# Kernel tuning notes

Measured on AMD Instinct MI355X. Metric: run time of the kernel, lower is better.

## Reference

```python
import jax, jax.numpy as jnp
import numpy as np

N_FEATURES = 512
DEPTH = 6
N_TREES = 64
D_OUT = 64
N_LEAVES = 2 ** DEPTH


def setup_inputs() -> dict:
    key = jax.random.key(0)
    k_x, k_w, k_b, k_leaf = jax.random.split(key, 4)
    B = 16384
    x = jax.random.normal(k_x, (B, N_FEATURES), dtype=jnp.float32)
    # depth independent Linear(n_features, n_trees) layers, stacked
    bound = 1.0 / np.sqrt(N_FEATURES)
    W = jax.random.uniform(k_w, (DEPTH, N_FEATURES, N_TREES), dtype=jnp.float32,
                           minval=-bound, maxval=bound)
    b = jax.random.uniform(k_b, (DEPTH, N_TREES), dtype=jnp.float32,
                           minval=-bound, maxval=bound)
    leaf_values = jax.random.normal(k_leaf, (N_TREES, N_LEAVES, D_OUT), dtype=jnp.float32)
    return {"x": x, "W": W, "b": b, "leaf_values": leaf_values}


def reference(x, W, b, leaf_values):
    B = x.shape[0]
    # split probabilities for all levels at once: [B, depth, n_trees]
    split_probs = jax.nn.sigmoid(jnp.einsum('bf,dft->bdt', x, W) + b)
    # bit of leaf index at each level: 0 -> take p (left), 1 -> take 1-p (right)
    leaf_ids = jnp.arange(N_LEAVES)
    # path_probs: [B, n_trees, n_leaves]; small fixed loop over depth levels
    path_probs = jnp.ones((B, N_TREES, N_LEAVES), dtype=x.dtype)
    for level in range(DEPTH):
        bit = (leaf_ids >> (DEPTH - level - 1)) & 1  # [n_leaves]
        p = split_probs[:, level, :, None]           # [B, n_trees, 1]
        path_probs = path_probs * jnp.where(bit == 0, p, 1.0 - p)
    # per-tree leaf combine then mean over trees
    out = jnp.einsum('btl,tld->bd', path_probs, leaf_values) / N_TREES
    return out
```

## Files before the change

### kernel.cpp

```cpp
#include <hip/hip_runtime.h>

#define BATCH   16384
#define NFEAT   512
#define NTREE   64
#define NDEPTH  6
#define NLEAF   64
#define NDOUT   64
#define NLOGIT  384

typedef float    f32x4  __attribute__((ext_vector_type(4)));
typedef short    short8 __attribute__((ext_vector_type(8)));
typedef _Float16 half8  __attribute__((ext_vector_type(8)));
typedef _Float16 h2     __attribute__((ext_vector_type(2)));

union U8 { unsigned short u[8]; short8 v; half8 h; };
union HP { _Float16 h[4]; ushort4 u; };
union HS { _Float16 h; unsigned short s; };
union H8 { h2 p[4]; half8 v; };

__device__ __forceinline__ unsigned short f2bf(float f) {
    union { float f; unsigned int u; } c; c.f = f;
    return (unsigned short)((c.u + 0x8000u) >> 16);
}

__device__ __forceinline__ unsigned short f2h(float f) {
    HS s; s.h = (_Float16)f; return s.s;
}

__device__ __forceinline__ void dma16(const void* g, void* l) {
    __builtin_amdgcn_global_load_lds(
        (const __attribute__((address_space(1))) unsigned int*)g,
        (__attribute__((address_space(3))) unsigned int*)l, 16, 0, 0);
}

__global__ __launch_bounds__(256) void prep(const float* __restrict__ leaf,
                                            const float* __restrict__ W,
                                            unsigned short* __restrict__ V3,
                                            unsigned short* __restrict__ Wt3) {
    __shared__ float T[64 * 65];
    const int tid = threadIdx.x;
    if (blockIdx.x < 64) {
        const int t = blockIdx.x;
        const float* src = leaf + (size_t)t * 4096;
        for (int j = 0; j < 4; ++j) {
            int idx = tid + 256 * j;
            int l = idx >> 4, d4 = idx & 15;
            float4 v = *(const float4*)(src + l * 64 + d4 * 4);
            T[l * 65 + d4 * 4 + 0] = v.x;
            T[l * 65 + d4 * 4 + 1] = v.y;
            T[l * 65 + d4 * 4 + 2] = v.z;
            T[l * 65 + d4 * 4 + 3] = v.w;
        }
        __syncthreads();
        #pragma unroll
        for (int jj = 0; jj < 2; ++jj) {
            int idx = tid + 256 * jj;
            int d = idx >> 3, o = idx & 7;
            int nt = d >> 4, l15 = d & 15;
            int ks = o >> 2, qd = o & 3;
            int lam = qd * 16 + l15;
            U8 u;
            #pragma unroll
            for (int j = 0; j < 8; ++j)
                u.u[j] = f2h(T[(o * 8 + j) * 65 + d] * 0.015625f);
            *(short8*)(V3 + (((size_t)t * 8 + nt * 2 + ks) * 64 + lam) * 8) = u.v;
        }
    } else {
        const int bid = blockIdx.x - 64;
        const int d = bid >> 4, f0 = (bid & 15) * 32;
        for (int j = 0; j < 2; ++j) {
            int idx = tid + 256 * j;
            int f = idx >> 4, c4 = idx & 15;
            float4 v = *(const float4*)(W + ((size_t)d * 512 + f0 + f) * 64 + c4 * 4);
            T[f * 65 + c4 * 4 + 0] = v.x;
            T[f * 65 + c4 * 4 + 1] = v.y;
            T[f * 65 + c4 * 4 + 2] = v.z;
            T[f * 65 + c4 * 4 + 3] = v.w;
        }
        __syncthreads();
        const int t = tid >> 2, c8 = tid & 3;
        U8 u;
        #pragma unroll
        for (int i = 0; i < 8; ++i) u.u[i] = f2bf(T[(c8 * 8 + i) * 65 + t]);
        int k0 = f0 + c8 * 8;
        int kb = k0 >> 6, ks = (k0 >> 5) & 1, qk = (k0 >> 3) & 3;
        int g  = d * 4 + (t >> 4);
        int lam = qk * 16 + (t & 15);
        *(short8*)(Wt3 + (((size_t)kb * 24 + g) * 2 + ks) * 512 + lam * 8) = u.v;
    }
}

__global__ __launch_bounds__(512) void fused(const float* __restrict__ x,
                                             const unsigned short* __restrict__ Wt3,
                                             const float* __restrict__ bias,
                                             const unsigned short* __restrict__ V3,
                                             float* __restrict__ out) {
    __shared__ char SM[64 * 1024];
    _Float16*       sp  = (_Float16*)SM;
    float*          As0 = (float*)(SM + 24 * 1024);
    float*          As1 = (float*)(SM + 32 * 1024);
    _Float16*       red = (_Float16*)(SM + 24 * 1024);

    const int tid  = threadIdx.x;
    const int w = tid >> 6, lane = tid & 63;
    const int quad = lane >> 4, l15 = lane & 15;
    const int r0 = blockIdx.x * 32;
    const int w3 = w * 3;

    f32x4 acc1[2][3];
    #pragma unroll
    for (int mt = 0; mt < 2; ++mt)
        #pragma unroll
        for (int nt = 0; nt < 3; ++nt)
            acc1[mt][nt] = (f32x4){0.f, 0.f, 0.f, 0.f};

    auto stageA = [&](float* buf, int kb) {
        int rl = w * 4 + (lane >> 4);
        const float* g = x + (size_t)(r0 + rl) * NFEAT + kb * 64
                       + (((lane & 15) ^ ((rl & 7) * 2)) * 4);
        dma16(g, (char*)buf + (size_t)w * 1024);
    };
    auto loadBF = [&](int kb, short8 (*bf)[2]) {
        #pragma unroll
        for (int nt = 0; nt < 3; ++nt)
            #pragma unroll
            for (int ks = 0; ks < 2; ++ks)
                bf[nt][ks] = *(const short8*)(Wt3 +
                    (((size_t)kb * 24 + w3 + nt) * 2 + ks) * 512 + lane * 8);
    };
    auto computeStep = [&](const float* buf, short8 (*bf)[2]) {
        short8 aF[2][2];
        #pragma unroll
        for (int mt = 0; mt < 2; ++mt) {
            int r = mt * 16 + l15;
            #pragma unroll
            for (int ks = 0; ks < 2; ++ks) {
                int cb = (ks * 8 + quad * 2) ^ ((r & 7) * 2);
                float4 f0 = *(const float4*)(buf + r * 64 + cb * 4);
                float4 f1 = *(const float4*)(buf + r * 64 + cb * 4 + 4);
                U8 u;
                u.u[0] = f2bf(f0.x); u.u[1] = f2bf(f0.y);
                u.u[2] = f2bf(f0.z); u.u[3] = f2bf(f0.w);
                u.u[4] = f2bf(f1.x); u.u[5] = f2bf(f1.y);
                u.u[6] = f2bf(f1.z); u.u[7] = f2bf(f1.w);
                aF[mt][ks] = u.v;
            }
        }
        #pragma unroll
        for (int mt = 0; mt < 2; ++mt)
            #pragma unroll
            for (int nt = 0; nt < 3; ++nt)
                #pragma unroll
                for (int ks = 0; ks < 2; ++ks)
                    acc1[mt][nt] = __builtin_amdgcn_mfma_f32_16x16x32_bf16(
                        aF[mt][ks], bf[nt][ks], acc1[mt][nt], 0, 0, 0);
    };

    short8 bC[3][2], bN[3][2];
    stageA(As0, 0);
    loadBF(0, bC);
    __syncthreads();
    #pragma unroll
    for (int kp = 0; kp < 4; ++kp) {
        int kb = kp * 2;
        stageA(As1, kb + 1);
        loadBF(kb + 1, bN);
        computeStep(As0, bC);
        __syncthreads();
        if (kb + 2 < 8) {
            stageA(As0, kb + 2);
            loadBF(kb + 2, bC);
        }
        computeStep(As1, bN);
        __syncthreads();
    }

    #pragma unroll
    for (int nt = 0; nt < 3; ++nt) {
        int n = w * 48 + nt * 16 + l15;
        float bv = bias[n];
        #pragma unroll
        for (int mt = 0; mt < 2; ++mt) {
            HP h;
            #pragma unroll
            for (int r = 0; r < 4; ++r) {
                float z = acc1[mt][nt][r] + bv;
                h.h[r] = (_Float16)(1.0f / (1.0f + __expf(-z)));
            }
            *(ushort4*)(sp + n * 32 + mt * 16 + quad * 4) = h.u;
        }
    }
    __syncthreads();

    const _Float16* V3h = (const _Float16*)V3;

    f32x4 acc[2][4];
    #pragma unroll
    for (int mt = 0; mt < 2; ++mt)
        #pragma unroll
        for (int nt = 0; nt < 4; ++nt)
            acc[mt][nt] = (f32x4){0.f, 0.f, 0.f, 0.f};

    auto loadB = [&](int t, half8 (*bf)[2]) {
        #pragma unroll
        for (int nt = 0; nt < 4; ++nt)
            #pragma unroll
            for (int ks = 0; ks < 2; ++ks)
                bf[nt][ks] = *(const half8*)(V3h +
                    (((size_t)t * 8 + nt * 2 + ks) * 64 + lane) * 8);
    };
    auto buildA = [&](int t, half8 (*af)[2]) {
        const _Float16 one = (_Float16)1.0f;
        #pragma unroll
        for (int mt = 0; mt < 2; ++mt) {
            int rl = mt * 16 + l15;
            _Float16 p0 = sp[(0 * 64 + t) * 32 + rl];
            _Float16 p1 = sp[(1 * 64 + t) * 32 + rl];
            _Float16 p2 = sp[(2 * 64 + t) * 32 + rl];
            _Float16 p3 = sp[(3 * 64 + t) * 32 + rl];
            _Float16 p4 = sp[(4 * 64 + t) * 32 + rl];
            _Float16 p5 = sp[(5 * 64 + t) * 32 + rl];
            _Float16 q1 = (quad & 2) ? (_Float16)(one - p1) : p1;
            _Float16 q2 = (quad & 1) ? (_Float16)(one - p2) : p2;
            _Float16 pre  = q1 * q2;
            _Float16 pre0 = p0 * pre;
            _Float16 pre1 = (_Float16)(one - p0) * pre;
            h2 t45 = { p4, (_Float16)(one - p4) };
            h2 t5  = { p5, (_Float16)(one - p5) };
            h2 a34 = (h2){ p3, p3 } * t45;
            _Float16 q3 = one - p3;
            h2 b34 = (h2){ q3, q3 } * t45;
            h2 w0 = (h2){ a34.x, a34.x } * t5;
            h2 w1 = (h2){ a34.y, a34.y } * t5;
            h2 w2 = (h2){ b34.x, b34.x } * t5;
            h2 w3 = (h2){ b34.y, b34.y } * t5;
            h2 P0 = { pre0, pre0 }, P1 = { pre1, pre1 };
            H8 a0, a1;
            a0.p[0] = P0 * w0; a0.p[1] = P0 * w1;
            a0.p[2] = P0 * w2; a0.p[3] = P0 * w3;
            a1.p[0] = P1 * w0; a1.p[1] = P1 * w1;
            a1.p[2] = P1 * w2; a1.p[3] = P1 * w3;
            af[mt][0] = a0.v;
            af[mt][1] = a1.v;
        }
    };

    half8 bA[4][2], bB[4][2], aF2[2][2];
    loadB(w * 8, bA);
    #pragma unroll 2
    for (int tl = 0; tl < 8; ++tl) {
        const int t = w * 8 + tl;
        half8 (*cur)[2] = (tl & 1) ? bB : bA;
        half8 (*nxt)[2] = (tl & 1) ? bA : bB;
        if (tl + 1 < 8) loadB(t + 1, nxt);
        buildA(t, aF2);
        #pragma unroll
        for (int mt = 0; mt < 2; ++mt)
            #pragma unroll
            for (int nt = 0; nt < 4; ++nt)
                #pragma unroll
                for (int ks = 0; ks < 2; ++ks)
                    acc[mt][nt] = __builtin_amdgcn_mfma_f32_16x16x32_f16(
                        aF2[mt][ks], cur[nt][ks], acc[mt][nt], 0, 0, 0);
    }

    #pragma unroll
    for (int mt = 0; mt < 2; ++mt)
        #pragma unroll
        for (int nt = 0; nt < 4; ++nt) {
            HP h;
            #pragma unroll
            for (int r = 0; r < 4; ++r) h.h[r] = (_Float16)acc[mt][nt][r];
            *(ushort4*)(red + (w * 64 + nt * 16 + l15) * 40 + mt * 16 + quad * 4) = h.u;
        }
    __syncthreads();
    {
        int b = tid >> 4;
        int doff = (tid & 15) * 4;
        float s[4];
        #pragma unroll
        for (int i = 0; i < 4; ++i) s[i] = 0.f;
        #pragma unroll
        for (int ww = 0; ww < 8; ++ww)
            #pragma unroll
            for (int i = 0; i < 4; ++i)
                s[i] += (float)red[(ww * 64 + doff + i) * 40 + b];
        float4 o0 = { s[0], s[1], s[2], s[3] };
        *(float4*)(out + (size_t)(r0 + b) * NDOUT + doff) = o0;
    }
}

extern "C" void kernel_launch(void* const* d_in, const int* in_sizes, int n_in,
                              void* d_out, int out_size, void* d_ws, size_t ws_size,
                              hipStream_t stream) {
    const float* x    = (const float*)d_in[0];
    const float* W    = (const float*)d_in[1];
    const float* bias = (const float*)d_in[2];
    const float* leaf = (const float*)d_in[3];
    float* out = (float*)d_out;

    unsigned short* V3  = (unsigned short*)d_ws;
    unsigned short* Wt3 = V3 + (size_t)NTREE * NLEAF * NDOUT;

    prep<<<160, 256, 0, stream>>>(leaf, W, V3, Wt3);
    fused<<<BATCH / 32, 512, 0, stream>>>(x, Wt3, bias, (const unsigned short*)V3, out);
}
```

Measured before the change: 101.5 us.

## Load x tiles directly into registers instead of staging through LDS

Replaces the global-to-LDS DMA staging of the x tile, and the LDS reads that followed it, with direct per-lane float4 global loads into double-buffered registers. This removes the two __syncthreads per k-step and the LDS round trip. In exchange, all 8 waves now redundantly load the same 32x64 x rows from global memory or L2, and register pressure rises from the extra float4 buffers.

```diff
diff --git a/kernel.cpp b/kernel.cpp
--- a/kernel.cpp
+++ b/kernel.cpp
@@ -25,12 +25,6 @@
 
 __device__ __forceinline__ unsigned short f2h(float f) {
     HS s; s.h = (_Float16)f; return s.s;
-}
-
-__device__ __forceinline__ void dma16(const void* g, void* l) {
-    __builtin_amdgcn_global_load_lds(
-        (const __attribute__((address_space(1))) unsigned int*)g,
-        (__attribute__((address_space(3))) unsigned int*)l, 16, 0, 0);
 }
 
 __global__ __launch_bounds__(256) void prep(const float* __restrict__ leaf,
@@ -97,8 +91,6 @@
                                              float* __restrict__ out) {
     __shared__ char SM[64 * 1024];
     _Float16*       sp  = (_Float16*)SM;
-    float*          As0 = (float*)(SM + 24 * 1024);
-    float*          As1 = (float*)(SM + 32 * 1024);
     _Float16*       red = (_Float16*)(SM + 24 * 1024);
 
     const int tid  = threadIdx.x;
@@ -114,13 +106,18 @@
         for (int nt = 0; nt < 3; ++nt)
             acc1[mt][nt] = (f32x4){0.f, 0.f, 0.f, 0.f};
 
-    auto stageA = [&](float* buf, int kb) {
-        int rl = w * 4 + (lane >> 4);
-        const float* g = x + (size_t)(r0 + rl) * NFEAT + kb * 64
-                       + (((lane & 15) ^ ((rl & 7) * 2)) * 4);
-        dma16(g, (char*)buf + (size_t)w * 1024);
-    };
-    auto loadBF = [&](int kb, short8 (*bf)[2]) {
+    auto loadA = [&](int kb, float4 (*pa)[2], float4 (*pb)[2]) {
+        #pragma unroll
+        for (int mt = 0; mt < 2; ++mt)
+            #pragma unroll
+            for (int ks = 0; ks < 2; ++ks) {
+                const float* g = x + (size_t)(r0 + mt * 16 + l15) * NFEAT
+                               + kb * 64 + ks * 32 + quad * 8;
+                pa[mt][ks] = *(const float4*)(g);
+                pb[mt][ks] = *(const float4*)(g + 4);
+            }
+    };
+    auto loadBv = [&](int kb, short8 (*bf)[2]) {
         #pragma unroll
         for (int nt = 0; nt < 3; ++nt)
             #pragma unroll
@@ -128,24 +125,19 @@
                 bf[nt][ks] = *(const short8*)(Wt3 +
                     (((size_t)kb * 24 + w3 + nt) * 2 + ks) * 512 + lane * 8);
     };
-    auto computeStep = [&](const float* buf, short8 (*bf)[2]) {
+    auto computeStep = [&](float4 (*pa)[2], float4 (*pb)[2], short8 (*bf)[2]) {
         short8 aF[2][2];
         #pragma unroll
-        for (int mt = 0; mt < 2; ++mt) {
-            int r = mt * 16 + l15;
+        for (int mt = 0; mt < 2; ++mt)
             #pragma unroll
             for (int ks = 0; ks < 2; ++ks) {
-                int cb = (ks * 8 + quad * 2) ^ ((r & 7) * 2);
-                float4 f0 = *(const float4*)(buf + r * 64 + cb * 4);
-                float4 f1 = *(const float4*)(buf + r * 64 + cb * 4 + 4);
                 U8 u;
-                u.u[0] = f2bf(f0.x); u.u[1] = f2bf(f0.y);
-                u.u[2] = f2bf(f0.z); u.u[3] = f2bf(f0.w);
-                u.u[4] = f2bf(f1.x); u.u[5] = f2bf(f1.y);
-                u.u[6] = f2bf(f1.z); u.u[7] = f2bf(f1.w);
+                u.u[0] = f2bf(pa[mt][ks].x); u.u[1] = f2bf(pa[mt][ks].y);
+                u.u[2] = f2bf(pa[mt][ks].z); u.u[3] = f2bf(pa[mt][ks].w);
+                u.u[4] = f2bf(pb[mt][ks].x); u.u[5] = f2bf(pb[mt][ks].y);
+                u.u[6] = f2bf(pb[mt][ks].z); u.u[7] = f2bf(pb[mt][ks].w);
                 aF[mt][ks] = u.v;
             }
-        }
         #pragma unroll
         for (int mt = 0; mt < 2; ++mt)
             #pragma unroll
@@ -156,23 +148,21 @@
                         aF[mt][ks], bf[nt][ks], acc1[mt][nt], 0, 0, 0);
     };
 
+    float4 rAa[2][2], rAb[2][2], rBa[2][2], rBb[2][2];
     short8 bC[3][2], bN[3][2];
-    stageA(As0, 0);
-    loadBF(0, bC);
-    __syncthreads();
+    loadA(0, rAa, rAb);
+    loadBv(0, bC);
     #pragma unroll
     for (int kp = 0; kp < 4; ++kp) {
         int kb = kp * 2;
-        stageA(As1, kb + 1);
-        loadBF(kb + 1, bN);
-        computeStep(As0, bC);
-        __syncthreads();
+        loadA(kb + 1, rBa, rBb);
+        loadBv(kb + 1, bN);
+        computeStep(rAa, rAb, bC);
         if (kb + 2 < 8) {
-            stageA(As0, kb + 2);
-            loadBF(kb + 2, bC);
-        }
-        computeStep(As1, bN);
-        __syncthreads();
+            loadA(kb + 2, rAa, rAb);
+            loadBv(kb + 2, bC);
+        }
+        computeStep(rBa, rBb, bN);
     }
 
     #pragma unroll
```

Measured after the change: 121.8 us. 20.0% more time.
